# Performance work log

Measured on AMD Instinct MI355X. Metric: run time of the kernel, lower is better.

Reference implementation:

```python
import math
import jax, jax.numpy as jnp
import numpy as np

B, M, N = 32, 64, 5000   # batch, multi_width (POMO rollouts), n_nodes
L, H, D, E = 100, 8, 16, 128  # local_size, head_num, qkv_dim, emb_dim


def setup_inputs() -> dict:
    key = jax.random.key(0)
    ks = jax.random.split(key, 10)
    return {
        "dist": jax.random.uniform(ks[0], (B, M, N), jnp.float32),
        "theta": jax.random.uniform(ks[1], (B, M, N), jnp.float32, minval=-math.pi, maxval=math.pi),
        "ninf_mask": jnp.zeros((B, M, N), jnp.float32),
        "W_init": jax.random.normal(ks[2], (E, 2), jnp.float32) * 0.1,
        "b_init": jax.random.normal(ks[3], (E,), jnp.float32) * 0.1,
        "cur_token": jax.random.uniform(ks[4], (E,), jnp.float32, minval=-1.0, maxval=1.0),
        "Wq": jax.random.normal(ks[5], (H * D, E), jnp.float32) * 0.05,
        "Wk": jax.random.normal(ks[6], (H * D, E), jnp.float32) * 0.05,
        "Wv": jax.random.normal(ks[7], (H * D, E), jnp.float32) * 0.05,
        "Wc": jax.random.normal(ks[8], (E, H * D), jnp.float32) * 0.05,
        "bc": jax.random.normal(ks[9], (E,), jnp.float32) * 0.05,
    }


def _positional_signal():
    # transformer sinusoidal encoding over the L gathered neighbors (E even -> no pad)
    num_ts = E // 2
    log_inc = math.log(10000.0) / max(num_ts - 1, 1)
    inv_ts = jnp.exp(jnp.arange(num_ts, dtype=jnp.float32) * -log_inc)
    pos = jnp.arange(L, dtype=jnp.float32)
    scaled = pos[:, None] * inv_ts[None, :]            # [L, E/2]
    return jnp.concatenate([jnp.sin(scaled), jnp.cos(scaled)], axis=1)  # [L, E]


def reference(dist, theta, ninf_mask, W_init, b_init, cur_token, Wq, Wk, Wv, Wc, bc):
    # mask out infeasible nodes (dist - (-inf) = +inf pushes them out of top-k)
    d = dist - ninf_mask                               # [B, M, N]
    neg_vals, idx = jax.lax.top_k(-d, L)               # smallest-L distances
    sorted_dist = -neg_vals                            # [B, M, L] ascending
    sorted_mask = jnp.take_along_axis(ninf_mask, idx, axis=-1)
    norm = sorted_dist.max(axis=-1, keepdims=True) + 1e-6
    sorted_dist = sorted_dist / norm
    sorted_theta = jnp.take_along_axis(theta, idx, axis=-1)
    sdt = jnp.stack([sorted_dist, sorted_theta], axis=-1)   # [B, M, L, 2]

    init_k = sdt @ W_init.T + b_init + _positional_signal()  # [B, M, L, E]

    # current-token query is a single shared learned vector -> q is [H, D]
    q = (Wq @ cur_token).reshape(H, D)
    kh = (init_k @ Wk.T).reshape(B, M, L, H, D)
    vh = (init_k @ Wv.T).reshape(B, M, L, H, D)

    score = jnp.einsum('hd,bmlhd->bhml', q, kh) / jnp.sqrt(jnp.float32(D))
    score = score + sorted_mask[:, None, :, :]              # rank3 ninf mask
    w = jax.nn.softmax(score, axis=-1)                      # [B, H, M, L]
    att = jnp.einsum('bhml,bmlhd->bmhd', w, vh).reshape(B, M, H * D)
    mh = att @ Wc.T + bc                                    # [B, M, E]

    score2 = jnp.einsum('bme,bmle->bml', mh, init_k) / jnp.sqrt(jnp.float32(E))

    # scatter local scores back into full [B, M, N]
    bi = jnp.arange(B)[:, None, None]
    mi = jnp.arange(M)[None, :, None]
    out = jnp.zeros((B, M, N), jnp.float32).at[bi, mi, idx].set(score2)
    return out
```

## Files before the change

### kernel.cpp

```cpp
#include <hip/hip_runtime.h>
#include <math.h>

#define B_ 32
#define M_ 64
#define N_ 5000
#define L_ 100
#define H_ 8
#define D_ 16
#define E_ 128
#define NBIN 1024
#define NI4 1250
#define NT 256

#define OFF_POSQ  0
#define OFF_C0    800
#define OFF_C1    808
#define OFF_C2    816
#define OFF_PV0   824
#define OFF_PV1   952
#define OFF_PVB   1080
#define OFF_WC0   1208
#define OFF_WC1   1336
#define OFF_WCB   1464
#define OFF_SB    1592
#define OFF_PCB   1596
#define OFF_PV    1696
#define OFF_PCT   14496

__device__ __forceinline__ int vbin(float v) {
  if (!(v >= 0.f)) return 0;
  if (v >= 1.0f) return NBIN - 1;
  return (int)(v * (float)NBIN);
}
__device__ __forceinline__ unsigned int umap(float v) {
  unsigned int b = __float_as_uint(v);
  return (b & 0x80000000u) ? ~b : (b | 0x80000000u);
}
__device__ __forceinline__ float unmap(unsigned int u) {
  unsigned int b = (u & 0x80000000u) ? (u ^ 0x80000000u) : ~u;
  return __uint_as_float(b);
}
#define HMAPA(b) ((((b) & 3) << 8) | ((b) >> 2))

__global__ __launch_bounds__(128) void precomp(
    const float* __restrict__ Wq, const float* __restrict__ Wk,
    const float* __restrict__ cur, const float* __restrict__ Wi,
    const float* __restrict__ bi, const float* __restrict__ Wv,
    const float* __restrict__ Wc, const float* __restrict__ bc,
    float* __restrict__ ws)
{
  const int tid = threadIdx.x;
  const int blk = blockIdx.x;
  __shared__ float pr[E_];
  __shared__ float red[8];
  const int lane = tid & 63, wvv = tid >> 6;

  if (blk == 0) {
    float qsv = 0.f;
    for (int e = 0; e < E_; ++e) qsv = fmaf(Wq[tid * E_ + e], cur[e], qsv);
    float wk0=0,wk1=0,wkb=0,pv0=0,pv1=0,pvb=0,wc0=0,wc1=0,wcb=0;
    for (int e = 0; e < E_; ++e) {
      float wi0 = Wi[2*e], wi1 = Wi[2*e+1], bie = bi[e];
      float wk = Wk[tid*E_+e], wvx = Wv[tid*E_+e], wcc = Wc[e*(H_*D_)+tid];
      wk0=fmaf(wk,wi0,wk0);  wk1=fmaf(wk,wi1,wk1);  wkb=fmaf(wk,bie,wkb);
      pv0=fmaf(wvx,wi0,pv0); pv1=fmaf(wvx,wi1,pv1); pvb=fmaf(wvx,bie,pvb);
      wc0=fmaf(wcc,wi0,wc0); wc1=fmaf(wcc,wi1,wc1); wcb=fmaf(wcc,bie,wcb);
    }
    ws[OFF_PV0+tid]=pv0; ws[OFF_PV1+tid]=pv1; ws[OFF_PVB+tid]=pvb;
    ws[OFF_WC0+tid]=wc0; ws[OFF_WC1+tid]=wc1; ws[OFF_WCB+tid]=wcb;
    float c0 = qsv*wk0, c1 = qsv*wk1, c2 = qsv*wkb;
    for (int off = 1; off < 16; off <<= 1) {
      c0 += __shfl_xor(c0, off, 16); c1 += __shfl_xor(c1, off, 16); c2 += __shfl_xor(c2, off, 16);
    }
    if ((tid & 15) == 0) {
      int h = tid >> 4;
      ws[OFF_C0+h] = c0*0.25f; ws[OFF_C1+h] = c1*0.25f; ws[OFF_C2+h] = c2*0.25f;
    }
    float p0 = Wi[2*tid]*bc[tid], p1 = Wi[2*tid+1]*bc[tid], p2 = bi[tid]*bc[tid];
    for (int off = 32; off > 0; off >>= 1) {
      p0 += __shfl_xor(p0, off, 64); p1 += __shfl_xor(p1, off, 64); p2 += __shfl_xor(p2, off, 64);
    }
    if (lane == 0) { red[wvv*3+0]=p0; red[wvv*3+1]=p1; red[wvv*3+2]=p2; }
    __syncthreads();
    if (tid == 0) {
      ws[OFF_SB+0]=red[0]+red[3]; ws[OFF_SB+1]=red[1]+red[4]; ws[OFF_SB+2]=red[2]+red[5];
    }
  } else {
    const int l = blk - 1;
    const float log_inc = 0.14619588050755848f;
    {
      int j = tid & 63;
      float scaled = (float)l * expf(-(float)j * log_inc);
      pr[tid] = (tid < 64) ? sinf(scaled) : cosf(scaled);
    }
    __syncthreads();
    float qsv=0.f, pwk=0.f, accv=0.f, accc=0.f;
    for (int e = 0; e < E_; ++e) qsv = fmaf(Wq[tid*E_+e], cur[e], qsv);
    for (int e = 0; e < E_; ++e) {
      float p = pr[e];
      pwk  = fmaf(Wk[tid*E_+e], p, pwk);
      accv = fmaf(Wv[tid*E_+e], p, accv);
      accc = fmaf(Wc[e*(H_*D_)+tid], p, accc);
    }
    ws[OFF_PV  + l*(H_*D_) + tid] = accv;
    ws[OFF_PCT + tid*L_ + l] = accc;
    float pq = qsv * pwk;
    for (int off = 1; off < 16; off <<= 1) pq += __shfl_xor(pq, off, 16);
    if ((tid & 15) == 0) ws[OFF_POSQ + (tid>>4)*L_ + l] = pq * 0.25f;
    float pb = pr[tid] * bc[tid];
    for (int off = 32; off > 0; off >>= 1) pb += __shfl_xor(pb, off, 64);
    if (lane == 0) red[wvv] = pb;
    __syncthreads();
    if (tid == 0) ws[OFF_PCB + l] = red[0] + red[1];
  }
}

__global__ __launch_bounds__(NT, 8) void local_att_kernel(
    const float* __restrict__ dist, const float* __restrict__ theta,
    const float* __restrict__ ninf, const float* __restrict__ ws,
    float* __restrict__ out)
{
  __shared__ unsigned int hist[NBIN];
  __shared__ unsigned long long sel[128];
  __shared__ float sdv[128];
  __shared__ unsigned int idxs[128];
  __shared__ float stv[128], smv[128];
  __shared__ float att[H_ * D_];
  __shared__ unsigned int bitmap[160];
  __shared__ unsigned int hidx[256];
  __shared__ float hval[256];
  __shared__ unsigned int wsum[4];
  __shared__ unsigned int s_bstar, s_cumB, s_binc, s_cnt, s_chosen, s_cumb2;

  const int tid = threadIdx.x;
  const int lane = tid & 63, wv = tid >> 6;
  const size_t base = (size_t)blockIdx.x * N_;
  const float4* d4 = (const float4*)(dist + base);
  const float4* n4 = (const float4*)(ninf + base);

  for (int j = tid; j < NBIN; j += NT) hist[j] = 0u;
  if (tid < 128) sel[tid] = ~0ull;
  if (tid == 0) s_cnt = 0u;
  __syncthreads();

  unsigned int u[20];
#pragma unroll
  for (int t = 0; t < 5; ++t) {
    int i4 = tid + NT * t;
    if (i4 < NI4) {
      float4 dv = d4[i4], nv = n4[i4];
#pragma unroll
      for (int c = 0; c < 4; ++c) {
        float v = (&dv.x)[c] - (&nv.x)[c];
        u[4 * t + c] = umap(v);
        atomicAdd(&hist[HMAPA(vbin(v))], 1u);
      }
    }
  }
  __syncthreads();

  {
    unsigned int h4[4]; unsigned int s = 0;
#pragma unroll
    for (int k = 0; k < 4; ++k) { h4[k] = hist[(k << 8) | tid]; s += h4[k]; }
    unsigned int v = s;
#pragma unroll
    for (int off = 1; off < 64; off <<= 1) {
      unsigned int x = __shfl_up(v, off, 64);
      if (lane >= off) v += x;
    }
    if (lane == 63) wsum[wv] = v;
    __syncthreads();
    { unsigned int add = 0; for (int ww = 0; ww < wv; ++ww) add += wsum[ww]; v += add; }
    unsigned int cumBefore = v - s;
    if (cumBefore < (unsigned)L_ && v >= (unsigned)L_) {
      unsigned int c = cumBefore;
#pragma unroll
      for (int k = 0; k < 4; ++k) {
        unsigned int h = h4[k];
        if (c + h >= (unsigned)L_) { s_bstar = tid * 4 + k; s_cumB = c; s_binc = h; break; }
        c += h;
      }
    }
    __syncthreads();
  }
  const int bstar = (int)s_bstar;
  const bool fb = (s_cumB + s_binc > 128u);

  if (!fb) {
#pragma unroll
    for (int t = 0; t < 5; ++t) {
      int i4 = tid + NT * t;
      if (i4 < NI4) {
#pragma unroll
        for (int c = 0; c < 4; ++c) {
          unsigned int uu = u[4 * t + c];
          if (vbin(unmap(uu)) <= bstar) {
            unsigned int p = atomicAdd(&s_cnt, 1u);
            if (p < 128u) sel[p] = ((unsigned long long)uu << 16) | (unsigned)(4 * i4 + c);
          }
        }
      }
    }
  } else {
    unsigned long long prefix = 0ull;
    unsigned int Krem = L_;
    for (int pass = 0; pass < 6; ++pass) {
      const int shift = 40 - 8 * pass;
      hist[tid] = 0u;
      __syncthreads();
#pragma unroll
      for (int t = 0; t < 5; ++t) {
        int i4 = tid + NT * t;
        if (i4 < NI4) {
#pragma unroll
          for (int c = 0; c < 4; ++c) {
            unsigned long long key = ((unsigned long long)u[4 * t + c] << 16) | (unsigned)(4 * i4 + c);
            if ((key >> (shift + 8)) == prefix)
              atomicAdd(&hist[(unsigned)(key >> shift) & 0xFFu], 1u);
          }
        }
      }
      __syncthreads();
      unsigned int s = hist[tid];
      unsigned int v = s;
#pragma unroll
      for (int off = 1; off < 64; off <<= 1) {
        unsigned int x = __shfl_up(v, off, 64);
        if (lane >= off) v += x;
      }
      if (lane == 63) wsum[wv] = v;
      __syncthreads();
      { unsigned int add = 0; for (int ww = 0; ww < wv; ++ww) add += wsum[ww]; v += add; }
      unsigned int cb = v - s;
      if (cb < Krem && v >= Krem) { s_chosen = (unsigned)tid; s_cumb2 = cb; }
      __syncthreads();
      prefix = (prefix << 8) | s_chosen;
      Krem -= s_cumb2;
      __syncthreads();
    }
    const unsigned long long kpiv = prefix;
#pragma unroll
    for (int t = 0; t < 5; ++t) {
      int i4 = tid + NT * t;
      if (i4 < NI4) {
#pragma unroll
        for (int c = 0; c < 4; ++c) {
          unsigned long long key = ((unsigned long long)u[4 * t + c] << 16) | (unsigned)(4 * i4 + c);
          if (key <= kpiv) {
            unsigned int p = atomicAdd(&s_cnt, 1u);
            if (p < 128u) sel[p] = key;
          }
        }
      }
    }
  }
  __syncthreads();

  if (tid < 128) {
    unsigned long long ka = sel[tid];
    const bool valid = (ka != ~0ull);
    unsigned int ix = (unsigned int)(ka & 0xFFFFull);
    float th = 0.f, nm = 0.f;
    if (valid) { th = theta[base + ix]; nm = ninf[base + ix]; }
    int ra = 0;
#pragma unroll 8
    for (int j = 0; j < 128; ++j) ra += (sel[j] < ka) ? 1 : 0;
    if (valid) {
      sdv[ra] = unmap((unsigned int)(ka >> 16));
      idxs[ra] = ix;
      stv[ra] = th;
      smv[ra] = nm;
    }
  } else if (tid < 192) {
    for (int j = tid - 128; j < 160; j += 64) bitmap[j] = 0u;
  } else {
    for (int j = tid - 192; j < 256; j += 64) hidx[j] = 0xFFFFFFFFu;
  }
  __syncthreads();

  const float invn = 1.0f / (sdv[L_ - 1] + 1e-6f);
  if (tid < 128) {
    const int hh = tid >> 4, jj = tid & 15;
    float w7[7];
    float a0, a1;
    {
      const float c0 = ws[OFF_C0 + hh], c1 = ws[OFF_C1 + hh], c2 = ws[OFF_C2 + hh];
      float mx = -INFINITY;
#pragma unroll
      for (int k = 0; k < 7; ++k) {
        int l = jj + 16 * k;
        float scv = -INFINITY;
        if (l < L_)
          scv = fmaf(sdv[l] * invn, c0, fmaf(stv[l], c1, c2 + ws[OFF_POSQ + hh * L_ + l] + smv[l]));
        w7[k] = scv;
        mx = fmaxf(mx, scv);
      }
#pragma unroll
      for (int off = 1; off <= 8; off <<= 1) mx = fmaxf(mx, __shfl_xor(mx, off, 64));
      float sum = 0.f;
#pragma unroll
      for (int k = 0; k < 7; ++k) { float e = expf(w7[k] - mx); w7[k] = e; sum += e; }
#pragma unroll
      for (int off = 1; off <= 8; off <<= 1) sum += __shfl_xor(sum, off, 64);
      const float inv = 1.0f / sum;
      a0 = 0.f; a1 = 0.f;
#pragma unroll
      for (int k = 0; k < 7; ++k) {
        int l = jj + 16 * k; int lc = (l < L_) ? l : 0;
        float wgt = w7[k] * inv; w7[k] = wgt;
        a0 = fmaf(wgt, sdv[lc] * invn, a0);
        a1 = fmaf(wgt, stv[lc], a1);
      }
#pragma unroll
      for (int off = 1; off <= 8; off <<= 1) { a0 += __shfl_xor(a0, off, 64); a1 += __shfl_xor(a1, off, 64); }
    }
    {
      float part[16];
#pragma unroll
      for (int t = 0; t < 16; ++t) part[t] = 0.f;
#pragma unroll
      for (int k = 0; k < 7; ++k) {
        int l = jj + 16 * k;
        if (l < L_) {
          const float* pv = ws + OFF_PV + l * (H_ * D_) + hh * 16;
          float wgt = w7[k];
#pragma unroll
          for (int t = 0; t < 16; ++t) part[t] = fmaf(wgt, pv[t], part[t]);
        }
      }
#pragma unroll
      for (int off = 1; off <= 8; off <<= 1) {
#pragma unroll
        for (int t = 0; t < 16; ++t) part[t] += __shfl_xor(part[t], off, 64);
      }
#pragma unroll
      for (int t = 0; t < 16; ++t) {
        int hd = hh * 16 + t;
        att[hd] = fmaf(a0, ws[OFF_PV0 + hd], fmaf(a1, ws[OFF_PV1 + hd], ws[OFF_PVB + hd])) + part[t];
      }
    }
  }
  __syncthreads();

  float m0 = 0.f, m1 = 0.f, mb = 0.f;
  if (tid < 128) {
    float x0 = att[lane], x1 = att[lane + 64];
    m0 = fmaf(x0, ws[OFF_WC0 + lane], x1 * ws[OFF_WC0 + lane + 64]);
    m1 = fmaf(x0, ws[OFF_WC1 + lane], x1 * ws[OFF_WC1 + lane + 64]);
    mb = fmaf(x0, ws[OFF_WCB + lane], x1 * ws[OFF_WCB + lane + 64]);
#pragma unroll
    for (int off = 1; off < 64; off <<= 1) {
      m0 += __shfl_xor(m0, off, 64);
      m1 += __shfl_xor(m1, off, 64);
      mb += __shfl_xor(mb, off, 64);
    }
    m0 += ws[OFF_SB + 0]; m1 += ws[OFF_SB + 1]; mb += ws[OFF_SB + 2];
  }

  if (tid < L_) {
    float acc = ws[OFF_PCB + tid];
#pragma unroll 8
    for (int hd = 0; hd < H_ * D_; ++hd) acc = fmaf(att[hd], ws[OFF_PCT + hd * L_ + tid], acc);
    const float SC = 0.08838834764831845f;
    float s2v = (fmaf(sdv[tid] * invn, m0, fmaf(stv[tid], m1, mb)) + acc) * SC;
    unsigned int idx = idxs[tid];
    unsigned int p = idx & 255u;
    while (atomicCAS(&hidx[p], 0xFFFFFFFFu, idx) != 0xFFFFFFFFu) p = (p + 1) & 255u;
    hval[p] = s2v;
    atomicOr(&bitmap[idx >> 5], 1u << (idx & 31));
  }
  __syncthreads();

  float4* o4 = (float4*)(out + base);
#pragma unroll
  for (int t = 0; t < 5; ++t) {
    int i4 = tid + NT * t;
    if (i4 < NI4) {
      unsigned int wbits = (bitmap[i4 >> 3] >> ((i4 & 7) * 4)) & 0xFu;
      float4 o = make_float4(0.f, 0.f, 0.f, 0.f);
      if (wbits) {
#pragma unroll
        for (int c = 0; c < 4; ++c) {
          if ((wbits >> c) & 1u) {
            unsigned int idx = (unsigned int)(4 * i4 + c);
            unsigned int p = idx & 255u;
            while (hidx[p] != idx) p = (p + 1) & 255u;
            (&o.x)[c] = hval[p];
          }
        }
      }
      o4[i4] = o;
    }
  }
}

extern "C" void kernel_launch(void* const* d_in, const int* in_sizes, int n_in,
                              void* d_out, int out_size, void* d_ws, size_t ws_size,
                              hipStream_t stream) {
  const float* dist = (const float*)d_in[0];
  const float* theta = (const float*)d_in[1];
  const float* ninf = (const float*)d_in[2];
  const float* Wi   = (const float*)d_in[3];
  const float* bi   = (const float*)d_in[4];
  const float* cur  = (const float*)d_in[5];
  const float* Wq   = (const float*)d_in[6];
  const float* Wk   = (const float*)d_in[7];
  const float* Wv   = (const float*)d_in[8];
  const float* Wc   = (const float*)d_in[9];
  const float* bcv  = (const float*)d_in[10];
  float* out = (float*)d_out;
  float* ws  = (float*)d_ws;

  precomp<<<dim3(L_ + 1), dim3(128), 0, stream>>>(Wq, Wk, cur, Wi, bi, Wv, Wc, bcv, ws);
  local_att_kernel<<<dim3(B_ * M_), dim3(NT), 0, stream>>>(dist, theta, ninf, ws, out);
}
```

Baseline: 84.43 us.

## Split fused kernel into select/math/write stages with fixed-threshold candidate filter

Replaces the 1024-bin histogram pass with a single fixed threshold (0.032) that collects candidates directly into a 256-entry buffer. A radix-select fallback, which re-reads the inputs from global memory, handles the case where the count falls outside the range 100 to 256. The fused kernel becomes three kernels that pass sorted distances, theta, mask, indices and scores through scratch space in the output buffer. This removes the histogram atomics and prefix scan and shrinks the per-block footprint, at the cost of two extra launches and extra global traffic. The threshold is tuned to uniform distances with N=5000, so other inputs rely on the slower fallback.

After: 73.49 us. 13.0% less time.

```diff
diff --git a/kernel.cpp b/kernel.cpp
--- a/kernel.cpp
+++ b/kernel.cpp
@@ -8,9 +8,15 @@
 #define H_ 8
 #define D_ 16
 #define E_ 128
-#define NBIN 1024
 #define NI4 1250
-#define NT 256
+#define T0 0.032f
+#define CAP 256
+
+#define ST_SD  0
+#define ST_TH  128
+#define ST_SM  256
+#define ST_IX  384
+#define ST_S2  512
 
 #define OFF_POSQ  0
 #define OFF_C0    800
@@ -27,11 +33,6 @@
 #define OFF_PV    1696
 #define OFF_PCT   14496
 
-__device__ __forceinline__ int vbin(float v) {
-  if (!(v >= 0.f)) return 0;
-  if (v >= 1.0f) return NBIN - 1;
-  return (int)(v * (float)NBIN);
-}
 __device__ __forceinline__ unsigned int umap(float v) {
   unsigned int b = __float_as_uint(v);
   return (b & 0x80000000u) ? ~b : (b | 0x80000000u);
@@ -40,7 +41,6 @@
   unsigned int b = (u & 0x80000000u) ? (u ^ 0x80000000u) : ~u;
   return __uint_as_float(b);
 }
-#define HMAPA(b) ((((b) & 3) << 8) | ((b) >> 2))
 
 __global__ __launch_bounds__(128) void precomp(
     const float* __restrict__ Wq, const float* __restrict__ Wk,
@@ -115,22 +115,15 @@
   }
 }
 
-__global__ __launch_bounds__(NT, 8) void local_att_kernel(
+__global__ __launch_bounds__(128, 4) void k1_select(
     const float* __restrict__ dist, const float* __restrict__ theta,
-    const float* __restrict__ ninf, const float* __restrict__ ws,
-    float* __restrict__ out)
+    const float* __restrict__ ninf, float* __restrict__ out)
 {
-  __shared__ unsigned int hist[NBIN];
-  __shared__ unsigned long long sel[128];
-  __shared__ float sdv[128];
-  __shared__ unsigned int idxs[128];
-  __shared__ float stv[128], smv[128];
-  __shared__ float att[H_ * D_];
-  __shared__ unsigned int bitmap[160];
-  __shared__ unsigned int hidx[256];
-  __shared__ float hval[256];
-  __shared__ unsigned int wsum[4];
-  __shared__ unsigned int s_bstar, s_cumB, s_binc, s_cnt, s_chosen, s_cumb2;
+  __shared__ unsigned long long sel[CAP];
+  __shared__ unsigned int hist[256];
+  __shared__ unsigned int wsum[2];
+  __shared__ unsigned int s_cnt, s_chosen, s_cumb2;
+  __shared__ float s_nrm;
 
   const int tid = threadIdx.x;
   const int lane = tid & 63, wv = tid >> 6;
@@ -138,91 +131,51 @@
   const float4* d4 = (const float4*)(dist + base);
   const float4* n4 = (const float4*)(ninf + base);
 
-  for (int j = tid; j < NBIN; j += NT) hist[j] = 0u;
-  if (tid < 128) sel[tid] = ~0ull;
+  sel[tid] = ~0ull; sel[tid + 128] = ~0ull;
   if (tid == 0) s_cnt = 0u;
   __syncthreads();
 
-  unsigned int u[20];
-#pragma unroll
-  for (int t = 0; t < 5; ++t) {
-    int i4 = tid + NT * t;
+#pragma unroll 2
+  for (int t = 0; t < 10; ++t) {
+    int i4 = tid + 128 * t;
     if (i4 < NI4) {
       float4 dv = d4[i4], nv = n4[i4];
 #pragma unroll
       for (int c = 0; c < 4; ++c) {
         float v = (&dv.x)[c] - (&nv.x)[c];
-        u[4 * t + c] = umap(v);
-        atomicAdd(&hist[HMAPA(vbin(v))], 1u);
-      }
-    }
-  }
-  __syncthreads();
-
-  {
-    unsigned int h4[4]; unsigned int s = 0;
-#pragma unroll
-    for (int k = 0; k < 4; ++k) { h4[k] = hist[(k << 8) | tid]; s += h4[k]; }
-    unsigned int v = s;
-#pragma unroll
-    for (int off = 1; off < 64; off <<= 1) {
-      unsigned int x = __shfl_up(v, off, 64);
-      if (lane >= off) v += x;
-    }
-    if (lane == 63) wsum[wv] = v;
-    __syncthreads();
-    { unsigned int add = 0; for (int ww = 0; ww < wv; ++ww) add += wsum[ww]; v += add; }
-    unsigned int cumBefore = v - s;
-    if (cumBefore < (unsigned)L_ && v >= (unsigned)L_) {
-      unsigned int c = cumBefore;
-#pragma unroll
-      for (int k = 0; k < 4; ++k) {
-        unsigned int h = h4[k];
-        if (c + h >= (unsigned)L_) { s_bstar = tid * 4 + k; s_cumB = c; s_binc = h; break; }
-        c += h;
-      }
-    }
-    __syncthreads();
-  }
-  const int bstar = (int)s_bstar;
-  const bool fb = (s_cumB + s_binc > 128u);
-
-  if (!fb) {
-#pragma unroll
-    for (int t = 0; t < 5; ++t) {
-      int i4 = tid + NT * t;
-      if (i4 < NI4) {
-#pragma unroll
-        for (int c = 0; c < 4; ++c) {
-          unsigned int uu = u[4 * t + c];
-          if (vbin(unmap(uu)) <= bstar) {
-            unsigned int p = atomicAdd(&s_cnt, 1u);
-            if (p < 128u) sel[p] = ((unsigned long long)uu << 16) | (unsigned)(4 * i4 + c);
-          }
+        if (v < T0) {
+          unsigned int p = atomicAdd(&s_cnt, 1u);
+          if (p < CAP) sel[p] = ((unsigned long long)umap(v) << 16) | (unsigned)(4 * i4 + c);
         }
       }
     }
-  } else {
+  }
+  __syncthreads();
+  const unsigned int cnt = s_cnt;
+
+  if (cnt < (unsigned)L_ || cnt > (unsigned)CAP) {
     unsigned long long prefix = 0ull;
     unsigned int Krem = L_;
     for (int pass = 0; pass < 6; ++pass) {
       const int shift = 40 - 8 * pass;
-      hist[tid] = 0u;
+      hist[tid] = 0u; hist[tid + 128] = 0u;
       __syncthreads();
-#pragma unroll
-      for (int t = 0; t < 5; ++t) {
-        int i4 = tid + NT * t;
+      for (int t = 0; t < 10; ++t) {
+        int i4 = tid + 128 * t;
         if (i4 < NI4) {
+          float4 dv = d4[i4], nv = n4[i4];
 #pragma unroll
           for (int c = 0; c < 4; ++c) {
-            unsigned long long key = ((unsigned long long)u[4 * t + c] << 16) | (unsigned)(4 * i4 + c);
+            float v = (&dv.x)[c] - (&nv.x)[c];
+            unsigned long long key = ((unsigned long long)umap(v) << 16) | (unsigned)(4 * i4 + c);
             if ((key >> (shift + 8)) == prefix)
               atomicAdd(&hist[(unsigned)(key >> shift) & 0xFFu], 1u);
           }
         }
       }
       __syncthreads();
-      unsigned int s = hist[tid];
+      unsigned int s0 = hist[2 * tid], s1 = hist[2 * tid + 1];
+      unsigned int s = s0 + s1;
       unsigned int v = s;
 #pragma unroll
       for (int off = 1; off < 64; off <<= 1) {
@@ -231,90 +184,124 @@
       }
       if (lane == 63) wsum[wv] = v;
       __syncthreads();
-      { unsigned int add = 0; for (int ww = 0; ww < wv; ++ww) add += wsum[ww]; v += add; }
+      if (wv == 1) v += wsum[0];
       unsigned int cb = v - s;
-      if (cb < Krem && v >= Krem) { s_chosen = (unsigned)tid; s_cumb2 = cb; }
+      if (cb < Krem && v >= Krem) {
+        if (cb + s0 >= Krem) { s_chosen = 2u * tid;     s_cumb2 = cb; }
+        else                 { s_chosen = 2u * tid + 1; s_cumb2 = cb + s0; }
+      }
       __syncthreads();
       prefix = (prefix << 8) | s_chosen;
       Krem -= s_cumb2;
       __syncthreads();
     }
     const unsigned long long kpiv = prefix;
-#pragma unroll
-    for (int t = 0; t < 5; ++t) {
-      int i4 = tid + NT * t;
+    sel[tid] = ~0ull; sel[tid + 128] = ~0ull;
+    if (tid == 0) s_cnt = 0u;
+    __syncthreads();
+    for (int t = 0; t < 10; ++t) {
+      int i4 = tid + 128 * t;
       if (i4 < NI4) {
+        float4 dv = d4[i4], nv = n4[i4];
 #pragma unroll
         for (int c = 0; c < 4; ++c) {
-          unsigned long long key = ((unsigned long long)u[4 * t + c] << 16) | (unsigned)(4 * i4 + c);
+          float v = (&dv.x)[c] - (&nv.x)[c];
+          unsigned long long key = ((unsigned long long)umap(v) << 16) | (unsigned)(4 * i4 + c);
           if (key <= kpiv) {
             unsigned int p = atomicAdd(&s_cnt, 1u);
-            if (p < 128u) sel[p] = key;
+            if (p < CAP) sel[p] = key;
           }
         }
       }
     }
-  }
-  __syncthreads();
-
-  if (tid < 128) {
-    unsigned long long ka = sel[tid];
-    const bool valid = (ka != ~0ull);
-    unsigned int ix = (unsigned int)(ka & 0xFFFFull);
-    float th = 0.f, nm = 0.f;
-    if (valid) { th = theta[base + ix]; nm = ninf[base + ix]; }
-    int ra = 0;
+    __syncthreads();
+  }
+
+  {
+    unsigned long long ka = sel[tid], kb = sel[tid + 128];
+    const bool va = (ka != ~0ull), vb = (kb != ~0ull);
+    unsigned int ixa = (unsigned int)(ka & 0xFFFFull);
+    unsigned int ixb = (unsigned int)(kb & 0xFFFFull);
+    float tha = 0.f, nma = 0.f, thb = 0.f, nmb = 0.f;
+    if (va) { tha = theta[base + ixa]; nma = ninf[base + ixa]; }
+    if (vb) { thb = theta[base + ixb]; nmb = ninf[base + ixb]; }
+    int ra = 0, rb = 0;
 #pragma unroll 8
-    for (int j = 0; j < 128; ++j) ra += (sel[j] < ka) ? 1 : 0;
-    if (valid) {
-      sdv[ra] = unmap((unsigned int)(ka >> 16));
-      idxs[ra] = ix;
-      stv[ra] = th;
-      smv[ra] = nm;
-    }
-  } else if (tid < 192) {
-    for (int j = tid - 128; j < 160; j += 64) bitmap[j] = 0u;
-  } else {
-    for (int j = tid - 192; j < 256; j += 64) hidx[j] = 0xFFFFFFFFu;
-  }
-  __syncthreads();
-
-  const float invn = 1.0f / (sdv[L_ - 1] + 1e-6f);
-  if (tid < 128) {
+    for (int j = 0; j < CAP; ++j) {
+      unsigned long long kj = sel[j];
+      ra += (kj < ka) ? 1 : 0;
+      rb += (kj < kb) ? 1 : 0;
+    }
+    float sda = unmap((unsigned int)(ka >> 16));
+    float sdb = unmap((unsigned int)(kb >> 16));
+    if (va && ra == 99) s_nrm = sda;
+    if (vb && rb == 99) s_nrm = sdb;
+    __syncthreads();
+    const float invn = 1.0f / (s_nrm + 1e-6f);
+    if (va && ra < L_) {
+      out[base + ST_SD + ra] = sda * invn;
+      out[base + ST_TH + ra] = tha;
+      out[base + ST_SM + ra] = nma;
+      out[base + ST_IX + ra] = __uint_as_float(ixa);
+    }
+    if (vb && rb < L_) {
+      out[base + ST_SD + rb] = sdb * invn;
+      out[base + ST_TH + rb] = thb;
+      out[base + ST_SM + rb] = nmb;
+      out[base + ST_IX + rb] = __uint_as_float(ixb);
+    }
+  }
+}
+
+__global__ __launch_bounds__(128, 4) void k2_math(
+    const float* __restrict__ ws, float* __restrict__ out)
+{
+  __shared__ float sdv[128], stv[128], smv[128];
+  __shared__ float att[H_ * D_];
+
+  const int tid = threadIdx.x;
+  const size_t base = (size_t)blockIdx.x * N_;
+
+  if (tid < L_) {
+    sdv[tid] = out[base + ST_SD + tid];
+    stv[tid] = out[base + ST_TH + tid];
+    smv[tid] = out[base + ST_SM + tid];
+  }
+  __syncthreads();
+
+  {
     const int hh = tid >> 4, jj = tid & 15;
     float w7[7];
     float a0, a1;
-    {
-      const float c0 = ws[OFF_C0 + hh], c1 = ws[OFF_C1 + hh], c2 = ws[OFF_C2 + hh];
-      float mx = -INFINITY;
-#pragma unroll
-      for (int k = 0; k < 7; ++k) {
-        int l = jj + 16 * k;
-        float scv = -INFINITY;
-        if (l < L_)
-          scv = fmaf(sdv[l] * invn, c0, fmaf(stv[l], c1, c2 + ws[OFF_POSQ + hh * L_ + l] + smv[l]));
-        w7[k] = scv;
-        mx = fmaxf(mx, scv);
-      }
-#pragma unroll
-      for (int off = 1; off <= 8; off <<= 1) mx = fmaxf(mx, __shfl_xor(mx, off, 64));
-      float sum = 0.f;
-#pragma unroll
-      for (int k = 0; k < 7; ++k) { float e = expf(w7[k] - mx); w7[k] = e; sum += e; }
-#pragma unroll
-      for (int off = 1; off <= 8; off <<= 1) sum += __shfl_xor(sum, off, 64);
-      const float inv = 1.0f / sum;
-      a0 = 0.f; a1 = 0.f;
-#pragma unroll
-      for (int k = 0; k < 7; ++k) {
-        int l = jj + 16 * k; int lc = (l < L_) ? l : 0;
-        float wgt = w7[k] * inv; w7[k] = wgt;
-        a0 = fmaf(wgt, sdv[lc] * invn, a0);
-        a1 = fmaf(wgt, stv[lc], a1);
-      }
-#pragma unroll
-      for (int off = 1; off <= 8; off <<= 1) { a0 += __shfl_xor(a0, off, 64); a1 += __shfl_xor(a1, off, 64); }
-    }
+    const float c0 = ws[OFF_C0 + hh], c1 = ws[OFF_C1 + hh], c2 = ws[OFF_C2 + hh];
+    float mx = -INFINITY;
+#pragma unroll
+    for (int k = 0; k < 7; ++k) {
+      int l = jj + 16 * k;
+      float scv = -INFINITY;
+      if (l < L_)
+        scv = fmaf(sdv[l], c0, fmaf(stv[l], c1, c2 + ws[OFF_POSQ + hh * L_ + l] + smv[l]));
+      w7[k] = scv;
+      mx = fmaxf(mx, scv);
+    }
+#pragma unroll
+    for (int off = 1; off <= 8; off <<= 1) mx = fmaxf(mx, __shfl_xor(mx, off, 64));
+    float sum = 0.f;
+#pragma unroll
+    for (int k = 0; k < 7; ++k) { float e = expf(w7[k] - mx); w7[k] = e; sum += e; }
+#pragma unroll
+    for (int off = 1; off <= 8; off <<= 1) sum += __shfl_xor(sum, off, 64);
+    const float inv = 1.0f / sum;
+    a0 = 0.f; a1 = 0.f;
+#pragma unroll
+    for (int k = 0; k < 7; ++k) {
+      int l = jj + 16 * k; int lc = (l < L_) ? l : 0;
+      float wgt = w7[k] * inv; w7[k] = wgt;
+      a0 = fmaf(wgt, sdv[lc], a0);
+      a1 = fmaf(wgt, stv[lc], a1);
+    }
+#pragma unroll
+    for (int off = 1; off <= 8; off <<= 1) { a0 += __shfl_xor(a0, off, 64); a1 += __shfl_xor(a1, off, 64); }
     {
       float part[16];
 #pragma unroll
@@ -343,8 +330,9 @@
   }
   __syncthreads();
 
-  float m0 = 0.f, m1 = 0.f, mb = 0.f;
-  if (tid < 128) {
+  float m0, m1, mb;
+  {
+    const int lane = tid & 63;
     float x0 = att[lane], x1 = att[lane + 64];
     m0 = fmaf(x0, ws[OFF_WC0 + lane], x1 * ws[OFF_WC0 + lane + 64]);
     m1 = fmaf(x0, ws[OFF_WC1 + lane], x1 * ws[OFF_WC1 + lane + 64]);
@@ -360,22 +348,42 @@
 
   if (tid < L_) {
     float acc = ws[OFF_PCB + tid];
-#pragma unroll 8
+#pragma unroll 16
     for (int hd = 0; hd < H_ * D_; ++hd) acc = fmaf(att[hd], ws[OFF_PCT + hd * L_ + tid], acc);
     const float SC = 0.08838834764831845f;
-    float s2v = (fmaf(sdv[tid] * invn, m0, fmaf(stv[tid], m1, mb)) + acc) * SC;
-    unsigned int idx = idxs[tid];
-    unsigned int p = idx & 255u;
-    while (atomicCAS(&hidx[p], 0xFFFFFFFFu, idx) != 0xFFFFFFFFu) p = (p + 1) & 255u;
-    hval[p] = s2v;
-    atomicOr(&bitmap[idx >> 5], 1u << (idx & 31));
+    out[base + ST_S2 + tid] = (fmaf(sdv[tid], m0, fmaf(stv[tid], m1, mb)) + acc) * SC;
+  }
+}
+
+__global__ __launch_bounds__(256, 4) void k3_write(float* __restrict__ out)
+{
+  __shared__ unsigned int bitmap[160];
+  __shared__ unsigned int hidx[256];
+  __shared__ float hval[256];
+
+  const int tid = threadIdx.x;
+  const size_t base = (size_t)blockIdx.x * N_;
+
+  unsigned int myidx = 0u; float myval = 0.f;
+  if (tid < L_) {
+    myidx = __float_as_uint(out[base + ST_IX + tid]);
+    myval = out[base + ST_S2 + tid];
+  }
+  hidx[tid] = 0xFFFFFFFFu;
+  if (tid < 160) bitmap[tid] = 0u;
+  __syncthreads();
+  if (tid < L_) {
+    unsigned int p = myidx & 255u;
+    while (atomicCAS(&hidx[p], 0xFFFFFFFFu, myidx) != 0xFFFFFFFFu) p = (p + 1) & 255u;
+    hval[p] = myval;
+    atomicOr(&bitmap[myidx >> 5], 1u << (myidx & 31));
   }
   __syncthreads();
 
   float4* o4 = (float4*)(out + base);
 #pragma unroll
   for (int t = 0; t < 5; ++t) {
-    int i4 = tid + NT * t;
+    int i4 = tid + 256 * t;
     if (i4 < NI4) {
       unsigned int wbits = (bitmap[i4 >> 3] >> ((i4 & 7) * 4)) & 0xFu;
       float4 o = make_float4(0.f, 0.f, 0.f, 0.f);
@@ -413,5 +421,7 @@
   float* ws  = (float*)d_ws;
 
   precomp<<<dim3(L_ + 1), dim3(128), 0, stream>>>(Wq, Wk, cur, Wi, bi, Wv, Wc, bcv, ws);
-  local_att_kernel<<<dim3(B_ * M_), dim3(NT), 0, stream>>>(dist, theta, ninf, ws, out);
-}
+  k1_select<<<dim3(B_ * M_), dim3(128), 0, stream>>>(dist, theta, ninf, out);
+  k2_math<<<dim3(B_ * M_), dim3(128), 0, stream>>>(ws, out);
+  k3_write<<<dim3(B_ * M_), dim3(256), 0, stream>>>(out);
+}
```
